# Kernel optimization log

Measured on AMD Instinct MI355X. Metric: run time of the kernel, lower is better.

Reference implementation:

```python
import jax, jax.numpy as jnp
import numpy as np

B = 131072
NUM_MODS = 6
NUM_PREDS = 30
CLS_TH = 2.0
CLS_IGNORE = 0.2
MGN = 0.2
CLS_COEF = 1.0
REG_COEF = 1.0


def setup_inputs() -> dict:
    key = jax.random.key(0)
    k1, k2, k3 = jax.random.split(key, 3)
    reg = jax.random.normal(k1, (B, NUM_MODS, NUM_PREDS, 2), jnp.float32)
    cls = jax.random.normal(k2, (B, NUM_MODS), jnp.float32)
    gt_preds = jax.random.normal(k3, (B, NUM_PREDS, 2), jnp.float32)
    has_preds = jnp.ones((B, NUM_PREDS), dtype=bool)
    return {"reg": reg, "cls": cls, "gt_preds": gt_preds, "has_preds": has_preds}


def _loss(reg, cls, gt, has):
    # ---------------- PredLoss (LaneGCN cls + reg loss) ----------------
    hasf = has.astype(jnp.float32)
    last = hasf + 0.1 * jnp.arange(NUM_PREDS, dtype=jnp.float32) / float(NUM_PREDS)
    last_idcs = jnp.argmax(last, axis=1)                      # [B]
    max_last = jnp.max(last, axis=1)
    valid = max_last > 1.0                                    # [B] rows kept by `mask`

    # distance of each mode's last-valid point to gt last-valid point
    reg_last = jnp.take_along_axis(reg, last_idcs[:, None, None, None], axis=2)[:, :, 0, :]  # [B,6,2]
    gt_last = jnp.take_along_axis(gt, last_idcs[:, None, None], axis=1)[:, 0, :]             # [B,2]
    dist = jnp.sqrt(((reg_last - gt_last[:, None, :]) ** 2).sum(-1))                          # [B,6]

    min_idcs = jnp.argmin(dist, axis=1)                       # [B]
    min_dist = jnp.min(dist, axis=1)

    cls_min = jnp.take_along_axis(cls, min_idcs[:, None], axis=1)  # [B,1]
    mgn = cls_min - cls                                            # [B,6]
    m01 = (min_dist < CLS_TH)[:, None] & ((dist - min_dist[:, None]) > CLS_IGNORE) & valid[:, None]
    cls_mask = m01 & (mgn < MGN)
    num_cls = cls_mask.sum()
    cls_loss = CLS_COEF * (MGN * num_cls.astype(jnp.float32) - jnp.where(cls_mask, mgn, 0.0).sum())

    # SmoothL1 (beta=1, reduction='sum') over best mode, masked by has & valid
    reg_best = jnp.take_along_axis(reg, min_idcs[:, None, None, None], axis=1)[:, 0]  # [B,30,2]
    diff = reg_best - gt
    ad = jnp.abs(diff)
    sl1 = jnp.where(ad < 1.0, 0.5 * diff * diff, ad - 0.5)
    w = (has & valid[:, None]).astype(jnp.float32)[..., None]  # [B,30,1]
    reg_loss = REG_COEF * (sl1 * w).sum()
    num_reg = (has & valid[:, None]).sum()

    loss = cls_loss / (num_cls.astype(jnp.float32) + 1e-10) + reg_loss / (num_reg.astype(jnp.float32) + 1e-10)

    # ---------------- heading (vectorized over scenes) ----------------
    gx, gy = gt[..., 0], gt[..., 1]                           # [B,30]
    fwd = jnp.arctan2(gy[:, 2:] - gy[:, 1:-1], gx[:, 2:] - gx[:, 1:-1])   # [B,28]
    bwd = jnp.arctan2(gy[:, 1:-1] - gy[:, :-2], gx[:, 1:-1] - gx[:, :-2]) # [B,28]
    head_tmp = jnp.rad2deg(fwd) + jnp.rad2deg(bwd)                         # [B,28]
    mid = jnp.where((fwd == 0.0) | (bwd == 0.0), head_tmp, head_tmp / 2.0)
    head0 = jnp.rad2deg(jnp.arctan2(gy[:, 1] - gy[:, 0], gx[:, 1] - gx[:, 0]))
    headL = jnp.rad2deg(jnp.arctan2(gy[:, -1] - gy[:, -2], gx[:, -1] - gx[:, -2]))
    head = jnp.concatenate([head0[:, None], mid, headL[:, None]], axis=1)  # [B,30]
    moving = jnp.sqrt(((gt[:, 0, :] - gt[:, -1, :]) ** 2).sum(-1)) > 2.0
    head = jnp.where(moving[:, None], head, 0.0)

    # ---------------- rotated dist_error (per-timestep 2x2 rotation) ----------------
    de0 = jnp.abs(gt[:, None, :, :] - reg)                    # [B,6,30,2] L1Loss(reduction='none')
    theta = jnp.deg2rad(-head)                                # [B,30]
    c = jnp.cos(theta)[:, None, :]                            # [B,1,30]
    s = jnp.sin(theta)[:, None, :]
    dx, dy = de0[..., 0], de0[..., 1]                         # [B,6,30]
    rx = c * dx - s * dy
    ry = s * dx + c * dy
    de = jnp.abs(jnp.stack([rx, ry], axis=-1))                # [B,6,30,2]

    top1 = jnp.argmax(cls, axis=1)                            # [B]
    de_top = jnp.take_along_axis(de, top1[:, None, None, None], axis=1)[:, 0]  # [B,30,2]

    ade6_x = de[..., 0].sum(); ade6_y = de[..., 1].sum()
    fde6_x = de[:, :, -1, 0].sum(); fde6_y = de[:, :, -1, 1].sum()
    ade1_x = de_top[..., 0].sum(); ade1_y = de_top[..., 1].sum()
    fde1_x = de_top[:, -1, 0].sum(); fde1_y = de_top[:, -1, 1].sum()

    Bn = de.shape[0]
    counts = jnp.array([
        NUM_MODS * Bn * NUM_PREDS,  # ade6_num
        NUM_MODS * Bn,              # fde6_num
        Bn * NUM_PREDS,             # ade1_num
        Bn,                         # fde1_num
    ], dtype=jnp.float32)

    return jnp.stack([
        loss, cls_loss, num_cls.astype(jnp.float32), reg_loss, num_reg.astype(jnp.float32),
        ade6_x, ade6_y, fde6_x, fde6_y, counts[0], counts[1],
        ade1_x, ade1_y, fde1_x, fde1_y, counts[2], counts[3],
    ])


def reference(reg, cls, gt_preds, has_preds):
    return _loss(reg, cls, gt_preds, has_preds)
```

## Files before the change

### kernel.cpp

```cpp
#include <hip/hip_runtime.h>
#include <math.h>

#define NROWS 131072
#define NMODS 6
#define NPREDS 30
#define RPG 4
#define NGROUPS (NROWS / RPG)
#define NBLK 2048
#define NWAVES (NBLK * 4)
#define GF4 (RPG * NMODS * 15)

#define ACC_SLOT(ws, i) ((float*)((char*)(ws) + (size_t)(i) * 256))

#define LGKM_WAIT() do { \
    __builtin_amdgcn_wave_barrier(); \
    __builtin_amdgcn_s_waitcnt(0xC07F); \
    __builtin_amdgcn_wave_barrier(); \
} while (0)

__device__ __forceinline__ float wave_reduce(float v) {
    v += __shfl_xor(v, 32);
    v += __shfl_xor(v, 16);
    v += __shfl_xor(v, 8);
    v += __shfl_xor(v, 4);
    v += __shfl_xor(v, 2);
    v += __shfl_xor(v, 1);
    return v;
}

__global__ __launch_bounds__(256) void loss_wave(
    const float* __restrict__ reg,
    const float* __restrict__ cls,
    const float* __restrict__ gt,
    const int* __restrict__ has,
    void* __restrict__ ws)
{
    const int tid  = threadIdx.x;
    const int lane = tid & 63;
    const int wid  = tid >> 6;
    const int gwave = blockIdx.x * 4 + wid;

    __shared__ float2 s_gt[4][RPG * NPREDS];
    __shared__ float2 s_ct[4][RPG * NPREDS];
    __shared__ float  s_red[4][12];

    float acc[12];
    #pragma unroll
    for (int i = 0; i < 12; ++i) acc[i] = 0.f;

    for (int g = gwave; g < NGROUPS; g += NWAVES) {
        const int rb = g * RPG;

        float4 gv = make_float4(0.f, 0.f, 0.f, 0.f);
        if (lane < 60) gv = ((const float4*)gt)[(size_t)rb * 15 + lane];
        int2 hv = make_int2(0, 0);
        if (lane < 60) hv = ((const int2*)has)[(size_t)rb * 15 + lane];

        const float4* reg4 = (const float4*)reg + (size_t)rb * 90;
        float4 rv[6];
        #pragma unroll
        for (int i = 0; i < 5; ++i) rv[i] = reg4[lane + 64 * i];
        if (lane < 40) rv[5] = reg4[lane + 320];

        unsigned long long bx = __ballot(lane < 60 && hv.x != 0);
        unsigned long long by = __ballot(lane < 60 && hv.y != 0);

        if (lane < 60) ((float4*)s_gt[wid])[lane] = gv;
        LGKM_WAIT();

        #pragma unroll
        for (int it = 0; it < 2; ++it) {
            int idx = lane + it * 64;
            if (idx < RPG * NPREDS) {
                int row = idx / NPREDS;
                int t   = idx - row * NPREDS;
                const float2* gp = s_gt[wid] + row * NPREDS;
                float2 g0 = gp[0], g29 = gp[NPREDS - 1];
                float mdx = g0.x - g29.x, mdy = g0.y - g29.y;
                bool moving = (mdx * mdx + mdy * mdy) > 4.0f;

                float2 cur = gp[t];
                float2 prv = gp[(t > 0) ? t - 1 : 0];
                float2 nxt = gp[(t < NPREDS - 1) ? t + 1 : NPREDS - 1];
                float fwd = atan2f(nxt.y - cur.y, nxt.x - cur.x);
                float bwd = atan2f(cur.y - prv.y, cur.x - prv.x);
                float head = (t == 0) ? fwd
                           : ((t == NPREDS - 1) ? bwd
                           : ((fwd == 0.f || bwd == 0.f) ? (fwd + bwd)
                                                         : 0.5f * (fwd + bwd)));
                if (!moving) head = 0.f;
                float s, c;
                __sincosf(-head, &s, &c);
                s_ct[wid][idx] = make_float2(c, s);
            }
        }

        unsigned metaval = 0u;
        if (lane < RPG) {
            unsigned ex = (unsigned)((bx >> (15 * lane)) & 0x7FFFull);
            unsigned ey = (unsigned)((by >> (15 * lane)) & 0x7FFFull);
            int le = ex ? 2 * (31 - __builtin_clz(ex)) : -1;
            int lo = ey ? 2 * (31 - __builtin_clz(ey)) + 1 : -1;
            int last = (le > lo) ? le : lo;
            if (last < 0) last = NPREDS - 1;
            bool valid = ((ex & ~1u) | ey) != 0u;

            float2 gl = s_gt[wid][lane * NPREDS + last];
            const float2* rr = (const float2*)reg + (size_t)(rb + lane) * 180;
            float dists[NMODS];
            #pragma unroll
            for (int m = 0; m < NMODS; ++m) {
                float2 rl = rr[m * NPREDS + last];
                float ax = rl.x - gl.x, ay = rl.y - gl.y;
                dists[m] = sqrtf(ax * ax + ay * ay);
            }
            float mind = dists[0]; int mini = 0;
            #pragma unroll
            for (int m = 1; m < NMODS; ++m)
                if (dists[m] < mind) { mind = dists[m]; mini = m; }

            const float2* cc = (const float2*)cls + (size_t)(rb + lane) * 3;
            float cv[NMODS];
            #pragma unroll
            for (int i = 0; i < 3; ++i) { float2 c = cc[i]; cv[2*i] = c.x; cv[2*i+1] = c.y; }
            float clsmin = cv[0];
            #pragma unroll
            for (int m = 1; m < NMODS; ++m) clsmin = (m == mini) ? cv[m] : clsmin;

            if (valid && (mind < 2.0f)) {
                #pragma unroll
                for (int m = 0; m < NMODS; ++m) {
                    float mgn = clsmin - cv[m];
                    if (((dists[m] - mind) > 0.2f) && (mgn < 0.2f)) {
                        acc[10] += 1.0f;
                        acc[9]  += mgn;
                    }
                }
            }
            float bc = cv[0]; int top1 = 0;
            #pragma unroll
            for (int m = 1; m < NMODS; ++m)
                if (cv[m] > bc) { bc = cv[m]; top1 = m; }

            if (valid)
                acc[11] += (float)(__builtin_popcount(ex) + __builtin_popcount(ey));

            metaval = (unsigned)mini | ((unsigned)top1 << 4) | (valid ? 256u : 0u);
        }
        LGKM_WAIT();

        #pragma unroll
        for (int i = 0; i < 6; ++i) {
            int k = lane + 64 * i;
            bool act = (i < 5) || (lane < 40);
            int kk = act ? k : 0;
            int row = kk / 90;
            int rem = kk - row * 90;
            int m   = rem / 15;
            int q   = rem - 15 * m;
            int t0  = 2 * q;

            unsigned mv = (unsigned)__shfl((int)metaval, row);
            unsigned ex = (unsigned)((bx >> (15 * row)) & 0x7FFFull);
            unsigned ey = (unsigned)((by >> (15 * row)) & 0x7FFFull);
            float4 gp = ((const float4*)s_gt[wid])[row * 15 + q];
            float4 sp = ((const float4*)s_ct[wid])[row * 15 + q];
            float4 v  = rv[i];

            unsigned mini = mv & 15u, top1 = (mv >> 4) & 15u;
            bool valid  = (mv & 256u) != 0u;
            bool isTop  = ((unsigned)m == top1);
            bool isBest = ((unsigned)m == mini) && valid;

            if (act) {
                {
                    float dx = fabsf(gp.x - v.x), dy = fabsf(gp.y - v.y);
                    float ax = fabsf(sp.x * dx - sp.y * dy);
                    float ay = fabsf(sp.y * dx + sp.x * dy);
                    acc[0] += ax; acc[1] += ay;
                    if (isTop) { acc[4] += ax; acc[5] += ay; }
                    if (isBest && ((ex >> q) & 1u)) {
                        float e0 = v.x - gp.x, e1 = v.y - gp.y;
                        float q0 = fabsf(e0), q1 = fabsf(e1);
                        acc[8] += (q0 < 1.f) ? (0.5f * e0 * e0) : (q0 - 0.5f);
                        acc[8] += (q1 < 1.f) ? (0.5f * e1 * e1) : (q1 - 0.5f);
                    }
                }
                {
                    float dx = fabsf(gp.z - v.z), dy = fabsf(gp.w - v.w);
                    float ax = fabsf(sp.z * dx - sp.w * dy);
                    float ay = fabsf(sp.w * dx + sp.z * dy);
                    acc[0] += ax; acc[1] += ay;
                    if (isTop) { acc[4] += ax; acc[5] += ay; }
                    if (q == 14) {
                        acc[2] += ax; acc[3] += ay;
                        if (isTop) { acc[6] += ax; acc[7] += ay; }
                    }
                    if (isBest && ((ey >> q) & 1u)) {
                        float e0 = v.z - gp.z, e1 = v.w - gp.w;
                        float q0 = fabsf(e0), q1 = fabsf(e1);
                        acc[8] += (q0 < 1.f) ? (0.5f * e0 * e0) : (q0 - 0.5f);
                        acc[8] += (q1 < 1.f) ? (0.5f * e1 * e1) : (q1 - 0.5f);
                    }
                }
            }
        }
        __builtin_amdgcn_wave_barrier();
    }

    #pragma unroll
    for (int i = 0; i < 12; ++i) acc[i] = wave_reduce(acc[i]);

    if (lane == 0) {
        #pragma unroll
        for (int i = 0; i < 12; ++i) s_red[wid][i] = acc[i];
    }
    __syncthreads();
    if (tid < 12) {
        float s = s_red[0][tid] + s_red[1][tid] + s_red[2][tid] + s_red[3][tid];
        atomicAdd(ACC_SLOT(ws, tid), s);
    }
}

__global__ void finalize(void* ws, float* __restrict__ out) {
    if (threadIdx.x == 0) {
        float nc = *ACC_SLOT(ws, 10), nr = *ACC_SLOT(ws, 11);
        float cls_loss = 0.2f * nc - *ACC_SLOT(ws, 9);
        float reg_loss = *ACC_SLOT(ws, 8);
        float loss = cls_loss / (nc + 1e-10f) + reg_loss / (nr + 1e-10f);
        out[0]  = loss;
        out[1]  = cls_loss;
        out[2]  = nc;
        out[3]  = reg_loss;
        out[4]  = nr;
        out[5]  = *ACC_SLOT(ws, 0);
        out[6]  = *ACC_SLOT(ws, 1);
        out[7]  = *ACC_SLOT(ws, 2);
        out[8]  = *ACC_SLOT(ws, 3);
        out[9]  = 23592960.0f;
        out[10] = 786432.0f;
        out[11] = *ACC_SLOT(ws, 4);
        out[12] = *ACC_SLOT(ws, 5);
        out[13] = *ACC_SLOT(ws, 6);
        out[14] = *ACC_SLOT(ws, 7);
        out[15] = 3932160.0f;
        out[16] = 131072.0f;
    }
}

extern "C" void kernel_launch(void* const* d_in, const int* in_sizes, int n_in,
                              void* d_out, int out_size, void* d_ws, size_t ws_size,
                              hipStream_t stream) {
    const float* reg = (const float*)d_in[0];
    const float* cls = (const float*)d_in[1];
    const float* gt  = (const float*)d_in[2];
    const int*   has = (const int*)d_in[3];
    float* out = (float*)d_out;

    hipMemsetAsync(d_ws, 0, 4096, stream);
    loss_wave<<<NBLK, 256, 0, stream>>>(reg, cls, gt, has, d_ws);
    finalize<<<1, 64, 0, stream>>>(d_ws, out);
}
```

Baseline: 328.8 us.

## Compute heading angles from registers via shuffles, sharing segment atan2 per lane

```diff
diff --git a/kernel.cpp b/kernel.cpp
--- a/kernel.cpp
+++ b/kernel.cpp
@@ -8,7 +8,6 @@
 #define NGROUPS (NROWS / RPG)
 #define NBLK 2048
 #define NWAVES (NBLK * 4)
-#define GF4 (RPG * NMODS * 15)
 
 #define ACC_SLOT(ws, i) ((float*)((char*)(ws) + (size_t)(i) * 256))
 
@@ -35,14 +34,17 @@
     const int* __restrict__ has,
     void* __restrict__ ws)
 {
-    const int tid  = threadIdx.x;
-    const int lane = tid & 63;
-    const int wid  = tid >> 6;
+    const int tid   = threadIdx.x;
+    const int lane  = tid & 63;
+    const int wid   = tid >> 6;
     const int gwave = blockIdx.x * 4 + wid;
 
-    __shared__ float2 s_gt[4][RPG * NPREDS];
-    __shared__ float2 s_ct[4][RPG * NPREDS];
+    __shared__ float4 s_gt[4][RPG * 15];
+    __shared__ float4 s_ct[4][RPG * 15];
     __shared__ float  s_red[4][12];
+
+    const int row = lane / 15;
+    const int q   = lane - row * 15;
 
     float acc[12];
     #pragma unroll
@@ -52,10 +54,11 @@
         const int rb = g * RPG;
 
         float4 gv = make_float4(0.f, 0.f, 0.f, 0.f);
-        if (lane < 60) gv = ((const float4*)gt)[(size_t)rb * 15 + lane];
-        int2 hv = make_int2(0, 0);
-        if (lane < 60) hv = ((const int2*)has)[(size_t)rb * 15 + lane];
-
+        int2   hv = make_int2(0, 0);
+        if (lane < 60) {
+            gv = ((const float4*)gt)[(size_t)rb * 15 + lane];
+            hv = ((const int2*)has)[(size_t)rb * 15 + lane];
+        }
         const float4* reg4 = (const float4*)reg + (size_t)rb * 90;
         float4 rv[6];
         #pragma unroll
@@ -65,53 +68,67 @@
         unsigned long long bx = __ballot(lane < 60 && hv.x != 0);
         unsigned long long by = __ballot(lane < 60 && hv.y != 0);
 
-        if (lane < 60) ((float4*)s_gt[wid])[lane] = gv;
+        unsigned ex = 0u, ey = 0u;
+        int last = NPREDS - 1;
+        bool valid = false;
+        float2 rl[NMODS];
+        float2 cc[3];
+        if (lane < RPG) {
+            ex = (unsigned)((bx >> (15 * lane)) & 0x7FFFull);
+            ey = (unsigned)((by >> (15 * lane)) & 0x7FFFull);
+            int le = ex ? 2 * (31 - __builtin_clz(ex)) : -1;
+            int lo = ey ? 2 * (31 - __builtin_clz(ey)) + 1 : -1;
+            last = (le > lo) ? le : lo;
+            if (last < 0) last = NPREDS - 1;
+            valid = ((ex & ~1u) | ey) != 0u;
+
+            const float2* rr = (const float2*)reg + (size_t)(rb + lane) * 180;
+            #pragma unroll
+            for (int m = 0; m < NMODS; ++m) rl[m] = rr[m * NPREDS + last];
+            const float2* cp = (const float2*)cls + (size_t)(rb + lane) * 3;
+            #pragma unroll
+            for (int i = 0; i < 3; ++i) cc[i] = cp[i];
+        }
+
+        float seg_e = atan2f(gv.w - gv.y, gv.z - gv.x);
+        float nx = __shfl(gv.x, lane + 1);
+        float ny = __shfl(gv.y, lane + 1);
+        float seg_o = atan2f(ny - gv.w, nx - gv.z);
+        float so_p  = __shfl(seg_o, lane - 1);
+
+        const int base = row * 15;
+        float g0x  = __shfl(gv.x, base),      g0y  = __shfl(gv.y, base);
+        float g29x = __shfl(gv.z, base + 14), g29y = __shfl(gv.w, base + 14);
+        float mdx = g0x - g29x, mdy = g0y - g29y;
+        const bool moving = (mdx * mdx + mdy * mdy) > 4.0f;
+
+        float head0 = (q == 0) ? seg_e
+                    : ((seg_e == 0.f || so_p == 0.f) ? (seg_e + so_p)
+                                                     : 0.5f * (seg_e + so_p));
+        float head1 = (q == 14) ? seg_e
+                    : ((seg_o == 0.f || seg_e == 0.f) ? (seg_o + seg_e)
+                                                      : 0.5f * (seg_o + seg_e));
+        if (!moving) { head0 = 0.f; head1 = 0.f; }
+        float c0, s0, c1, s1;
+        __sincosf(-head0, &s0, &c0);
+        __sincosf(-head1, &s1, &c1);
+
+        if (lane < 60) {
+            s_gt[wid][lane] = gv;
+            s_ct[wid][lane] = make_float4(c0, s0, c1, s1);
+        }
         LGKM_WAIT();
-
-        #pragma unroll
-        for (int it = 0; it < 2; ++it) {
-            int idx = lane + it * 64;
-            if (idx < RPG * NPREDS) {
-                int row = idx / NPREDS;
-                int t   = idx - row * NPREDS;
-                const float2* gp = s_gt[wid] + row * NPREDS;
-                float2 g0 = gp[0], g29 = gp[NPREDS - 1];
-                float mdx = g0.x - g29.x, mdy = g0.y - g29.y;
-                bool moving = (mdx * mdx + mdy * mdy) > 4.0f;
-
-                float2 cur = gp[t];
-                float2 prv = gp[(t > 0) ? t - 1 : 0];
-                float2 nxt = gp[(t < NPREDS - 1) ? t + 1 : NPREDS - 1];
-                float fwd = atan2f(nxt.y - cur.y, nxt.x - cur.x);
-                float bwd = atan2f(cur.y - prv.y, cur.x - prv.x);
-                float head = (t == 0) ? fwd
-                           : ((t == NPREDS - 1) ? bwd
-                           : ((fwd == 0.f || bwd == 0.f) ? (fwd + bwd)
-                                                         : 0.5f * (fwd + bwd)));
-                if (!moving) head = 0.f;
-                float s, c;
-                __sincosf(-head, &s, &c);
-                s_ct[wid][idx] = make_float2(c, s);
-            }
-        }
 
         unsigned metaval = 0u;
         if (lane < RPG) {
-            unsigned ex = (unsigned)((bx >> (15 * lane)) & 0x7FFFull);
-            unsigned ey = (unsigned)((by >> (15 * lane)) & 0x7FFFull);
-            int le = ex ? 2 * (31 - __builtin_clz(ex)) : -1;
-            int lo = ey ? 2 * (31 - __builtin_clz(ey)) + 1 : -1;
-            int last = (le > lo) ? le : lo;
-            if (last < 0) last = NPREDS - 1;
-            bool valid = ((ex & ~1u) | ey) != 0u;
-
-            float2 gl = s_gt[wid][lane * NPREDS + last];
-            const float2* rr = (const float2*)reg + (size_t)(rb + lane) * 180;
+            float4 gq = s_gt[wid][lane * 15 + (last >> 1)];
+            float glx = (last & 1) ? gq.z : gq.x;
+            float gly = (last & 1) ? gq.w : gq.y;
+
             float dists[NMODS];
             #pragma unroll
             for (int m = 0; m < NMODS; ++m) {
-                float2 rl = rr[m * NPREDS + last];
-                float ax = rl.x - gl.x, ay = rl.y - gl.y;
+                float ax = rl[m].x - glx, ay = rl[m].y - gly;
                 dists[m] = sqrtf(ax * ax + ay * ay);
             }
             float mind = dists[0]; int mini = 0;
@@ -119,10 +136,9 @@
             for (int m = 1; m < NMODS; ++m)
                 if (dists[m] < mind) { mind = dists[m]; mini = m; }
 
-            const float2* cc = (const float2*)cls + (size_t)(rb + lane) * 3;
             float cv[NMODS];
             #pragma unroll
-            for (int i = 0; i < 3; ++i) { float2 c = cc[i]; cv[2*i] = c.x; cv[2*i+1] = c.y; }
+            for (int i = 0; i < 3; ++i) { cv[2*i] = cc[i].x; cv[2*i+1] = cc[i].y; }
             float clsmin = cv[0];
             #pragma unroll
             for (int m = 1; m < NMODS; ++m) clsmin = (m == mini) ? cv[m] : clsmin;
@@ -147,30 +163,28 @@
 
             metaval = (unsigned)mini | ((unsigned)top1 << 4) | (valid ? 256u : 0u);
         }
-        LGKM_WAIT();
 
         #pragma unroll
         for (int i = 0; i < 6; ++i) {
             int k = lane + 64 * i;
             bool act = (i < 5) || (lane < 40);
             int kk = act ? k : 0;
-            int row = kk / 90;
-            int rem = kk - row * 90;
+            int rw  = kk / 90;
+            int rem = kk - rw * 90;
             int m   = rem / 15;
-            int q   = rem - 15 * m;
-            int t0  = 2 * q;
-
-            unsigned mv = (unsigned)__shfl((int)metaval, row);
-            unsigned ex = (unsigned)((bx >> (15 * row)) & 0x7FFFull);
-            unsigned ey = (unsigned)((by >> (15 * row)) & 0x7FFFull);
-            float4 gp = ((const float4*)s_gt[wid])[row * 15 + q];
-            float4 sp = ((const float4*)s_ct[wid])[row * 15 + q];
+            int qq  = rem - 15 * m;
+
+            unsigned mv  = (unsigned)__shfl((int)metaval, rw);
+            unsigned exr = (unsigned)((bx >> (15 * rw)) & 0x7FFFull);
+            unsigned eyr = (unsigned)((by >> (15 * rw)) & 0x7FFFull);
+            float4 gp = s_gt[wid][rw * 15 + qq];
+            float4 sp = s_ct[wid][rw * 15 + qq];
             float4 v  = rv[i];
 
             unsigned mini = mv & 15u, top1 = (mv >> 4) & 15u;
-            bool valid  = (mv & 256u) != 0u;
+            bool vld    = (mv & 256u) != 0u;
             bool isTop  = ((unsigned)m == top1);
-            bool isBest = ((unsigned)m == mini) && valid;
+            bool isBest = ((unsigned)m == mini) && vld;
 
             if (act) {
                 {
@@ -179,7 +193,7 @@
                     float ay = fabsf(sp.y * dx + sp.x * dy);
                     acc[0] += ax; acc[1] += ay;
                     if (isTop) { acc[4] += ax; acc[5] += ay; }
-                    if (isBest && ((ex >> q) & 1u)) {
+                    if (isBest && ((exr >> qq) & 1u)) {
                         float e0 = v.x - gp.x, e1 = v.y - gp.y;
                         float q0 = fabsf(e0), q1 = fabsf(e1);
                         acc[8] += (q0 < 1.f) ? (0.5f * e0 * e0) : (q0 - 0.5f);
@@ -192,11 +206,11 @@
                     float ay = fabsf(sp.w * dx + sp.z * dy);
                     acc[0] += ax; acc[1] += ay;
                     if (isTop) { acc[4] += ax; acc[5] += ay; }
-                    if (q == 14) {
+                    if (qq == 14) {
                         acc[2] += ax; acc[3] += ay;
                         if (isTop) { acc[6] += ax; acc[7] += ay; }
                     }
-                    if (isBest && ((ey >> q) & 1u)) {
+                    if (isBest && ((eyr >> qq) & 1u)) {
                         float e0 = v.z - gp.z, e1 = v.w - gp.w;
                         float q0 = fabsf(e0), q1 = fabsf(e1);
                         acc[8] += (q0 < 1.f) ? (0.5f * e0 * e0) : (q0 - 0.5f);
```

After: 304.5 us. 1.08x faster.
